# Kernel tuning notes

Hardware: AMD Instinct MI355X
Metric: run time of the kernel (lower is better)

Reference implementation:

```python
import jax, jax.numpy as jnp
import numpy as np

S, T, B = 128, 64, 64          # src_len, trg_len, batch
E, H, D, A, V = 512, 512, 1024, 256, 32000  # emb, enc_hid, dec_hid(=2H), attn, vocab
PAD = 0


def _p(key, shape, scale=0.02):
    return jax.random.normal(key, shape, dtype=jnp.float32) * scale


def setup_inputs() -> dict:
    key = jax.random.key(0)
    ks = jax.random.split(key, 20)
    return {
        'src': jax.random.randint(ks[0], (S, B), 0, V, dtype=jnp.int32),
        'trg': jax.random.randint(ks[1], (T, B), 0, V, dtype=jnp.int32),
        'enc_emb': _p(ks[2], (V, E)),
        'Wf_ih': _p(ks[3], (4 * H, E)), 'Wf_hh': _p(ks[4], (4 * H, H)), 'bf': jnp.zeros((4 * H,), jnp.float32),
        'Wb_ih': _p(ks[5], (4 * H, E)), 'Wb_hh': _p(ks[6], (4 * H, H)), 'bb': jnp.zeros((4 * H,), jnp.float32),
        'Wa': _p(ks[7], (A, 2 * H + D)), 'ba': jnp.zeros((A,), jnp.float32),
        'v': _p(ks[8], (A,)),
        'dec_emb': _p(ks[9], (V, E)),
        'Wd_ih': _p(ks[10], (4 * D, E + 2 * H)), 'Wd_hh': _p(ks[11], (4 * D, D)), 'bd': jnp.zeros((4 * D,), jnp.float32),
        'Wo': _p(ks[12], (V, 2 * H + D + E)), 'bo': jnp.zeros((V,), jnp.float32),
    }


def lstm_cell(x, h, c, W_ih, W_hh, b):
    # PyTorch gate order: i, f, g, o
    g = x @ W_ih.T + h @ W_hh.T + b
    i, f, gg, o = jnp.split(g, 4, axis=-1)
    c2 = jax.nn.sigmoid(f) * c + jax.nn.sigmoid(i) * jnp.tanh(gg)
    h2 = jax.nn.sigmoid(o) * jnp.tanh(c2)
    return h2, c2


def seq2seq_fwd(src, trg, enc_emb, Wf_ih, Wf_hh, bf, Wb_ih, Wb_hh, bb,
                Wa, ba, v, dec_emb, Wd_ih, Wd_hh, bd, Wo, bo):
    emb = enc_emb[src]                                   # [S,B,E]
    z = jnp.zeros((B, H), emb.dtype)

    def fstep(carry, x):
        h, c = lstm_cell(x, *carry, Wf_ih, Wf_hh, bf)
        return (h, c), h

    def bstep(carry, x):
        h, c = lstm_cell(x, *carry, Wb_ih, Wb_hh, bb)
        return (h, c), h

    (hf, cf), hs_f = jax.lax.scan(fstep, (z, z), emb)
    (hb, cb), hs_b = jax.lax.scan(bstep, (z, z), emb[::-1])
    enc_out = jnp.concatenate([hs_f, hs_b[::-1]], axis=-1)   # [S,B,2H]

    h0 = jnp.concatenate([hf, hb], axis=-1)              # [B,D]
    c0 = jnp.concatenate([cf, cb], axis=-1)

    mask = (src != PAD).T                                # [B,S]
    enc_bse = enc_out.transpose(1, 0, 2)                 # [B,S,2H]

    def dstep(carry, tok):
        h, c = carry
        emb_t = dec_emb[tok]                             # [B,E]
        hrep = jnp.broadcast_to(h[:, None, :], (B, S, D))
        energy = jnp.tanh(jnp.concatenate([hrep, enc_bse], -1) @ Wa.T + ba)  # [B,S,A]
        scores = energy @ v                              # [B,S]
        scores = jnp.where(mask, scores, jnp.float32(-1e10))
        a = jax.nn.softmax(scores, axis=1)
        ctx = jnp.einsum('bs,bse->be', a, enc_bse)       # [B,2H]
        x = jnp.concatenate([emb_t, ctx], axis=-1)
        h2, c2 = lstm_cell(x, h, c, Wd_ih, Wd_hh, bd)
        pred = jnp.concatenate([h2, ctx, emb_t], -1) @ Wo.T + bo  # [B,V]
        return (h2, c2), pred

    # teacher_forcing_ratio = 1.0 -> input at step t is trg[t-1]
    _, preds = jax.lax.scan(dstep, (h0, c0), trg[:-1])
    outputs = jnp.concatenate([jnp.zeros((1, B, V), preds.dtype), preds], axis=0)
    return outputs                                       # [T,B,V]


def reference(src, trg, enc_emb, Wf_ih, Wf_hh, bf, Wb_ih, Wb_hh, bb,
              Wa, ba, v, dec_emb, Wd_ih, Wd_hh, bd, Wo, bo):
    return seq2seq_fwd(src, trg, enc_emb, Wf_ih, Wf_hh, bf, Wb_ih, Wb_hh, bb,
                       Wa, ba, v, dec_emb, Wd_ih, Wd_hh, bd, Wo, bo)
```

## Files before the change

kernel.cpp:

```cpp
#include <hip/hip_runtime.h>

#define SLEN  128
#define BATCH 64
#define EMB   512
#define HID   512
#define DDEC  1024
#define ATT   256
#define VOC   32000
#define TSTEPS 63
#define SLOT  1024

typedef _Float16 f16x4 __attribute__((ext_vector_type(4)));
typedef _Float16 f16x8 __attribute__((ext_vector_type(8)));
typedef float    f32x4 __attribute__((ext_vector_type(4)));

union HQ  { unsigned long long q[2]; f16x8 v; };
union HP  { _Float16 h[2]; unsigned u; };
union HP4 { _Float16 h[4]; f16x4 v4; unsigned long long u; };

__device__ __forceinline__ float sigmoidf_(float x) { return 1.0f / (1.0f + __expf(-x)); }
__device__ __forceinline__ float tanhf_(float x)    { return 1.0f - 2.0f / (__expf(2.0f * x) + 1.0f); }

__device__ __forceinline__ void st_u32(void* p, unsigned v) {
    __hip_atomic_store((unsigned*)p, v, __ATOMIC_RELAXED, __HIP_MEMORY_SCOPE_AGENT);
}
__device__ __forceinline__ void st_u64(void* p, unsigned long long v) {
    __hip_atomic_store((unsigned long long*)p, v, __ATOMIC_RELAXED, __HIP_MEMORY_SCOPE_AGENT);
}
__device__ __forceinline__ unsigned long long ld_u64(const void* p) {
    return __hip_atomic_load((const unsigned long long*)p, __ATOMIC_RELAXED, __HIP_MEMORY_SCOPE_AGENT);
}
__device__ __forceinline__ void st_i32(int* p, int v) {
    __hip_atomic_store(p, v, __ATOMIC_RELAXED, __HIP_MEMORY_SCOPE_AGENT);
}
__device__ __forceinline__ int ld_i32(const int* p) {
    return __hip_atomic_load(p, __ATOMIC_RELAXED, __HIP_MEMORY_SCOPE_AGENT);
}

__device__ __forceinline__ void bar_arrive(int* flags, int myid, int epoch) {
    __syncthreads();
    if (threadIdx.x == 0) st_i32(flags + myid * SLOT, epoch);
}
__device__ __forceinline__ void bar_wait(int* flags, int nf, int epoch) {
    if ((int)threadIdx.x < 64) {
        bool done = false;
        while (!done) {
            bool ok = true;
            for (int i = threadIdx.x; i < nf; i += 64)
                ok = ok && (ld_i32(flags + i * SLOT) >= epoch);
            done = __all(ok);
            if (!done) __builtin_amdgcn_s_sleep(1);
        }
    }
    __syncthreads();
}

__global__ __launch_bounds__(256) void init_convert(
    const int* __restrict__ src, const int* __restrict__ trg,
    const float* __restrict__ enc_emb, const float* __restrict__ dec_emb,
    const float* __restrict__ Wf_ih, const float* __restrict__ Wf_hh,
    const float* __restrict__ Wb_ih, const float* __restrict__ Wb_hh,
    const float* __restrict__ Wa, const float* __restrict__ Wd_ih, const float* __restrict__ Wd_hh,
    float* __restrict__ out0,
    _Float16* __restrict__ Wenc16, _Float16* __restrict__ Wd16, _Float16* __restrict__ Wa16,
    _Float16* __restrict__ emb_src16, _Float16* __restrict__ predA,
    float* __restrict__ c_enc, _Float16* __restrict__ h16_enc, int* __restrict__ bar_ws)
{
    long idx = (long)blockIdx.x * 256 + threadIdx.x;
    if (idx < 2048000L) { out0[idx] = 0.f; return; }
    idx -= 2048000L;
    if (idx < 4194304L) {
        int dir = (int)(idx >> 21);
        int rem = (int)(idx & ((1 << 21) - 1));
        int rr = rem >> 10, c = rem & 1023;
        int d = rr >> 2, qg = rr & 3;
        const float* Wih = dir ? Wb_ih : Wf_ih;
        const float* Whh = dir ? Wb_hh : Wf_hh;
        float v = (c < 512) ? Wih[(long)(qg * 512 + d) * 512 + c]
                            : Whh[(long)(qg * 512 + d) * 512 + (c - 512)];
        Wenc16[idx] = (_Float16)v; return;
    }
    idx -= 4194304L;
    if (idx < 10485760L) {
        int rr = (int)(idx / 2560), c = (int)(idx % 2560);
        int d = rr >> 2, qg = rr & 3;
        float v = (c < 1536) ? Wd_ih[(long)(qg * 1024 + d) * 1536 + c]
                             : Wd_hh[(long)(qg * 1024 + d) * 1024 + (c - 1536)];
        Wd16[idx] = (_Float16)v; return;
    }
    idx -= 10485760L;
    if (idx < 262144L) {
        int rr = (int)(idx >> 10), c = (int)(idx & 1023);
        Wa16[idx] = (_Float16)Wa[(long)rr * 2048 + c]; return;
    }
    idx -= 262144L;
    if (idx < 4194304L) {
        int sb = (int)(idx >> 9), e = (int)(idx & 511);
        int tok = src[sb];
        emb_src16[idx] = (_Float16)enc_emb[(long)tok * 512 + e]; return;
    }
    idx -= 4194304L;
    if (idx < 2064384L) {
        int rI = (int)(idx >> 9), e = (int)(idx & 511);
        int tok = trg[rI];
        predA[(long)(64 + rI) * 2560 + 2048 + e] = (_Float16)dec_emb[(long)tok * 512 + e]; return;
    }
    idx -= 2064384L;
    if (idx < 65536L) { c_enc[idx] = 0.f; return; }
    idx -= 65536L;
    if (idx < 65536L) { h16_enc[idx] = (_Float16)0.f; return; }
    idx -= 65536L;
    if (idx < 655360L) { bar_ws[idx] = 0; }
}

__global__ __launch_bounds__(256, 1) void enc_coop(
    const _Float16* __restrict__ Wenc16, const _Float16* __restrict__ emb_src16,
    _Float16* __restrict__ h16_enc, float* __restrict__ c_enc,
    const float* __restrict__ bf, const float* __restrict__ bb,
    _Float16* __restrict__ enc_out16, int* __restrict__ bar_ws)
{
    __shared__ _Float16 Wl[32768];
    __shared__ float gbuf[32][34];

    const int t = threadIdx.x, lane = t & 63, wv = t >> 6;
    const int blk = blockIdx.x;
    const int g = blk >> 6, wb = blk & 63;
    const int dir = g >> 1, bh = g & 1;
    const int r16 = lane & 15, kg = lane >> 4;
    int* eflags = bar_ws + (384 + g * 64) * SLOT;

    #pragma unroll
    for (int i = 0; i < 16; ++i) {
        int h0 = (i * 256 + t) * 8;
        int kc = h0 >> 10;
        int rem = h0 & 1023;
        int gt2 = rem >> 9, l = (rem >> 3) & 63;
        f16x8 v = *(const f16x8*)(Wenc16 +
            ((size_t)(dir * 2048 + wb * 32 + gt2 * 16 + (l & 15))) * 1024 + (l >> 4) * 8 + kc * 32);
        *(f16x8*)&Wl[h0] = v;
    }

    const float* bias = dir ? bb : bf;
    const int pb = t & 31, dp = t >> 5;
    const int dl0 = dp * 2;
    float bias2[2][4], creg2[2] = {0.f, 0.f};
    if (t < 128) {
        #pragma unroll
        for (int j = 0; j < 2; ++j)
            #pragma unroll
            for (int q = 0; q < 4; ++q)
                bias2[j][q] = bias[q * 512 + wb * 8 + dl0 + j];
    }
    __syncthreads();

    for (int s = 0; s < SLEN; ++s) {
        const int par = s & 1;
        const int s_eff = dir ? (127 - s) : s;
        const int gt = wv & 1, mb = wv >> 1;
        const int arow = bh * 32 + mb * 16 + r16;
        const _Float16* Ax = emb_src16 + ((size_t)(s_eff * 64 + arow)) * 512 + kg * 8;
        const unsigned long long* Hq =
            (const unsigned long long*)(h16_enc + ((size_t)((par * 2 + dir) * 64 + arow)) * 512);
        f32x4 acc = {};
        #pragma unroll 4
        for (int kc = 0; kc < 16; ++kc) {
            f16x8 bw = *(const f16x8*)&Wl[kc * 1024 + gt * 512 + lane * 8];
            f16x8 a  = *(const f16x8*)(Ax + kc * 32);
            acc = __builtin_amdgcn_mfma_f32_16x16x32_f16(a, bw, acc, 0, 0, 0);
        }
        #pragma unroll 4
        for (int kc = 0; kc < 16; ++kc) {
            f16x8 bw = *(const f16x8*)&Wl[(16 + kc) * 1024 + gt * 512 + lane * 8];
            HQ hq;
            hq.q[0] = ld_u64(Hq + kc * 8 + kg * 2);
            hq.q[1] = ld_u64(Hq + kc * 8 + kg * 2 + 1);
            acc = __builtin_amdgcn_mfma_f32_16x16x32_f16(hq.v, bw, acc, 0, 0, 0);
        }
        #pragma unroll
        for (int rI = 0; rI < 4; ++rI)
            gbuf[gt * 16 + (lane & 15)][mb * 16 + kg * 4 + rI] = acc[rI];
        __syncthreads();
        if (t < 128) {
            HP hp;
            #pragma unroll
            for (int j = 0; j < 2; ++j) {
                const int dl = dl0 + j;
                float g0 = gbuf[dl * 4 + 0][pb] + bias2[j][0];
                float g1 = gbuf[dl * 4 + 1][pb] + bias2[j][1];
                float g2 = gbuf[dl * 4 + 2][pb] + bias2[j][2];
                float g3 = gbuf[dl * 4 + 3][pb] + bias2[j][3];
                float c2 = sigmoidf_(g1) * creg2[j] + sigmoidf_(g0) * tanhf_(g2);
                float h2 = sigmoidf_(g3) * tanhf_(c2);
                creg2[j] = c2;
                hp.h[j] = (_Float16)h2;
            }
            const int bglob = bh * 32 + pb;
            const int d0 = wb * 8 + dl0;
            st_u32((void*)(h16_enc + ((size_t)((par ^ 1) * 2 + dir) * 64 + bglob) * 512 + d0), hp.u);
            *(unsigned*)(enc_out16 + ((size_t)s_eff * 64 + bglob) * 1024 + dir * 512 + d0) = hp.u;
        }
        bar_arrive(eflags, wb, s + 1);
        bar_wait(eflags, 64, s + 1);
    }
    if (t < 128) {
        const int bglob = bh * 32 + pb;
        const int d0 = wb * 8 + dl0;
        c_enc[((size_t)dir * 64 + bglob) * 512 + d0] = creg2[0];
        c_enc[((size_t)dir * 64 + bglob) * 512 + d0 + 1] = creg2[1];
    }
}

__global__ __launch_bounds__(256, 1) void dec_coop(
    const _Float16* __restrict__ Wd16, const _Float16* __restrict__ Wa16,
    const float* __restrict__ bd, const float* __restrict__ vvec,
    const int* __restrict__ src, const _Float16* __restrict__ enc_part16,
    const _Float16* __restrict__ enc_out16, const float* __restrict__ c_enc,
    _Float16* __restrict__ predA, int* __restrict__ bar_ws)
{
    __shared__ float gbuf[16][68];
    __shared__ float ha[256], sv[256], sc[128], esum[256], red[4];

    const int t = threadIdx.x, lane = t & 63, wv = t >> 6;
    const int r16 = lane & 15, kg = lane >> 4;
    const int blk = blockIdx.x;
    int* cf  = bar_ws;
    int* hs  = bar_ws + 64 * SLOT;
    int* hf0 = bar_ws + 320 * SLOT;

    if (blk < 64) {
        const int wb = blk;
        sv[t] = vvec[t];
        {
            const int d0 = t * 4;
            const size_t rbase = (d0 < 512) ? (size_t)(127 * 64 + wb) * 1024
                                            : (size_t)(0 * 64 + wb) * 1024;
            HP4 o;
            o.h[0] = enc_out16[rbase + d0];
            o.h[1] = enc_out16[rbase + d0 + 1];
            o.h[2] = enc_out16[rbase + d0 + 2];
            o.h[3] = enc_out16[rbase + d0 + 3];
            st_u64((void*)(predA + (size_t)wb * 2560 + d0), o.u);
        }
        bar_arrive(hf0, wb, 1);
        for (int tt = 0; tt < TSTEPS; ++tt) {
            if (tt == 0) bar_wait(hf0, 64, 1); else bar_wait(hs, 256, tt);
            {
                const int base_m = wb & 48;
                const _Float16* Ahh = predA + ((size_t)(tt * 64 + base_m + r16)) * 2560 + kg * 8;
                f32x4 acc4[4] = {};
                #pragma unroll 4
                for (int kc = 0; kc < 32; ++kc) {
                    f16x8 a = *(const f16x8*)(Ahh + kc * 32);
                    #pragma unroll
                    for (int jj = 0; jj < 4; ++jj) {
                        f16x8 bw = *(const f16x8*)(Wa16 +
                            ((size_t)((wv * 4 + jj) * 16 + r16)) * 1024 + kg * 8 + kc * 32);
                        acc4[jj] = __builtin_amdgcn_mfma_f32_16x16x32_f16(a, bw, acc4[jj], 0, 0, 0);
                    }
                }
                if (kg == ((wb & 15) >> 2)) {
                    #pragma unroll
                    for (int jj = 0; jj < 4; ++jj)
                        ha[(wv * 4 + jj) * 16 + r16] = acc4[jj][wb & 3];
                }
            }
            __syncthreads();
            {
                const int s = t & 127, jh = t >> 7;
                const f16x8* ep = (const f16x8*)(enc_part16 + ((size_t)s * 64 + wb) * 256 + jh * 128);
                float acc = 0.f;
                #pragma unroll 2
                for (int j8 = 0; j8 < 16; ++j8) {
                    f16x8 e = ep[j8];
                    #pragma unroll
                    for (int u = 0; u < 8; ++u)
                        acc += tanhf_(ha[jh * 128 + j8 * 8 + u] + (float)e[u]) * sv[jh * 128 + j8 * 8 + u];
                }
                esum[t] = acc;
            }
            __syncthreads();
            if (t < 128) {
                float scv = esum[t] + esum[128 + t];
                scv = (src[t * 64 + wb] != 0) ? scv : -1e10f;
                sc[t] = scv;
                float v = scv;
                #pragma unroll
                for (int off = 32; off > 0; off >>= 1) v = fmaxf(v, __shfl_xor(v, off));
                if (lane == 0) red[t >> 6] = v;
            }
            __syncthreads();
            {
                const float mx = fmaxf(red[0], red[1]);
                if (t < 128) {
                    float e = __expf(sc[t] - mx);
                    sc[t] = e;
                    float v = e;
                    #pragma unroll
                    for (int off = 32; off > 0; off >>= 1) v += __shfl_xor(v, off);
                    if (lane == 0) red[2 + (t >> 6)] = v;
                }
            }
            __syncthreads();
            {
                const float inv = 1.0f / (red[2] + red[3]);
                float a0 = 0.f, a1 = 0.f, a2 = 0.f, a3 = 0.f;
                #pragma unroll 4
                for (int sI = 0; sI < 128; ++sI) {
                    float as = sc[sI] * inv;
                    f16x4 ev = *(const f16x4*)(enc_out16 + ((size_t)sI * 64 + wb) * 1024 + t * 4);
                    a0 += as * (float)ev[0]; a1 += as * (float)ev[1];
                    a2 += as * (float)ev[2]; a3 += as * (float)ev[3];
                }
                HP4 o;
                o.h[0] = (_Float16)a0; o.h[1] = (_Float16)a1;
                o.h[2] = (_Float16)a2; o.h[3] = (_Float16)a3;
                st_u64((void*)(predA + ((size_t)(64 + tt * 64 + wb)) * 2560 + 1024 + t * 4), o.u);
            }
            bar_arrive(cf, wb, tt + 1);
        }
    } else {
        const int gid = blk - 64;
        const int pb = t & 63;
        float bias2[2][4], creg2[2] = {0.f, 0.f};
        if (t < 128) {
            #pragma unroll
            for (int j = 0; j < 2; ++j) {
                const int dg = gid * 4 + (t >> 6) * 2 + j;
                #pragma unroll
                for (int q = 0; q < 4; ++q) bias2[j][q] = bd[q * 1024 + dg];
                creg2[j] = (dg < 512) ? c_enc[(size_t)pb * 512 + dg]
                                      : c_enc[(size_t)(64 + pb) * 512 + (dg - 512)];
            }
        }
        const _Float16* Bbase = Wd16 + (size_t)(gid * 16 + r16) * 2560 + kg * 8;
        for (int tt = 0; tt < TSTEPS; ++tt) {
            if (tt == 0) bar_wait(hf0, 64, 1); else bar_wait(hs, 256, tt);
            const int mb = wv;
            const _Float16* Ae = predA + ((size_t)(64 + tt * 64 + mb * 16 + r16)) * 2560 + kg * 8;
            const _Float16* Ah = predA + ((size_t)(tt * 64 + mb * 16 + r16)) * 2560 + kg * 8;
            f32x4 acc = {};
            #pragma unroll 4
            for (int kc = 0; kc < 16; ++kc) {
                f16x8 bw = *(const f16x8*)(Bbase + kc * 32);
                f16x8 a  = *(const f16x8*)(Ae + 2048 + kc * 32);
                acc = __builtin_amdgcn_mfma_f32_16x16x32_f16(a, bw, acc, 0, 0, 0);
            }
            #pragma unroll 4
            for (int kc = 0; kc < 32; ++kc) {
                f16x8 bw = *(const f16x8*)(Bbase + 1536 + kc * 32);
                f16x8 a  = *(const f16x8*)(Ah + kc * 32);
                acc = __builtin_amdgcn_mfma_f32_16x16x32_f16(a, bw, acc, 0, 0, 0);
            }
            bar_wait(cf, 64, tt + 1);
            #pragma unroll 4
            for (int kc = 0; kc < 32; ++kc) {
                f16x8 bw = *(const f16x8*)(Bbase + 512 + kc * 32);
                f16x8 a  = *(const f16x8*)(Ae + 1024 + kc * 32);
                acc = __builtin_amdgcn_mfma_f32_16x16x32_f16(a, bw, acc, 0, 0, 0);
            }
            #pragma unroll
            for (int rI = 0; rI < 4; ++rI)
                gbuf[lane & 15][mb * 16 + kg * 4 + rI] = acc[rI];
            __syncthreads();
            if (t < 128) {
                HP hp;
                #pragma unroll
                for (int j = 0; j < 2; ++j) {
                    const int dl = (t >> 6) * 2 + j;
                    float g0 = gbuf[dl * 4 + 0][pb] + bias2[j][0];
                    float g1 = gbuf[dl * 4 + 1][pb] + bias2[j][1];
                    float g2 = gbuf[dl * 4 + 2][pb] + bias2[j][2];
                    float g3 = gbuf[dl * 4 + 3][pb] + bias2[j][3];
                    float c2 = sigmoidf_(g1) * creg2[j] + sigmoidf_(g0) * tanhf_(g2);
                    float h2 = sigmoidf_(g3) * tanhf_(c2);
                    creg2[j] = c2;
                    hp.h[j] = (_Float16)h2;
                }
                st_u32((void*)(predA + ((size_t)(64 + tt * 64 + pb)) * 2560 + gid * 4 + (t >> 6) * 2), hp.u);
            }
            bar_arrive(hs, gid, tt + 1);
        }
    }
}

__global__ __launch_bounds__(64) void enc_step_mfma(
    const _Float16* __restrict__ Wenc16, const _Float16* __restrict__ emb_src16,
    _Float16* __restrict__ h16_enc, float* __restrict__ c_enc,
    const float* __restrict__ bf, const float* __restrict__ bb,
    _Float16* __restrict__ enc_out16, int s)
{
    __shared__ float gbuf[16 * 66];
    const int lane = threadIdx.x;
    const int blk = blockIdx.x;
    const int dir = blk >> 7, tile = blk & 127;
    const int par = s & 1;
    const int s_eff = dir ? (SLEN - 1 - s) : s;
    const int r16 = lane & 15, kg = lane >> 4;

    const _Float16* Bw = Wenc16 + ((size_t)(dir * 2048 + tile * 16 + r16)) * 1024 + kg * 8;
    const _Float16* Ax = emb_src16 + ((size_t)(s_eff * 64 + r16)) * 512 + kg * 8;
    const _Float16* Ah = h16_enc + ((size_t)((par * 2 + dir) * 64 + r16)) * 512 + kg * 8;

    f32x4 acc[4] = {};
    #pragma unroll 4
    for (int kc = 0; kc < 16; ++kc) {
        f16x8 bfr = *(const f16x8*)(Bw + kc * 32);
        #pragma unroll
        for (int m = 0; m < 4; ++m) {
            f16x8 a = *(const f16x8*)(Ax + kc * 32 + (size_t)m * 16 * 512);
            acc[m] = __builtin_amdgcn_mfma_f32_16x16x32_f16(a, bfr, acc[m], 0, 0, 0);
        }
    }
    #pragma unroll 4
    for (int kc = 0; kc < 16; ++kc) {
        f16x8 bfr = *(const f16x8*)(Bw + 512 + kc * 32);
        #pragma unroll
        for (int m = 0; m < 4; ++m) {
            f16x8 a = *(const f16x8*)(Ah + kc * 32 + (size_t)m * 16 * 512);
            acc[m] = __builtin_amdgcn_mfma_f32_16x16x32_f16(a, bfr, acc[m], 0, 0, 0);
        }
    }
    #pragma unroll
    for (int m = 0; m < 4; ++m)
        #pragma unroll
        for (int rI = 0; rI < 4; ++rI)
            gbuf[r16 * 66 + m * 16 + kg * 4 + rI] = acc[m][rI];
    __syncthreads();

    const float* bias = dir ? bb : bf;
    const int b = lane;
    #pragma unroll
    for (int dl = 0; dl < 4; ++dl) {
        const int d = tile * 4 + dl;
        float g0 = gbuf[(dl * 4 + 0) * 66 + b] + bias[d];
        float g1 = gbuf[(dl * 4 + 1) * 66 + b] + bias[512 + d];
        float g2 = gbuf[(dl * 4 + 2) * 66 + b] + bias[1024 + d];
        float g3 = gbuf[(dl * 4 + 3) * 66 + b] + bias[1536 + d];
        const size_t cur = ((size_t)(par * 2 + dir) * 64 + b) * 512 + d;
        const size_t nxt = ((size_t)((par ^ 1) * 2 + dir) * 64 + b) * 512 + d;
        float c2 = sigmoidf_(g1) * c_enc[cur] + sigmoidf_(g0) * tanhf_(g2);
        float h2 = sigmoidf_(g3) * tanhf_(c2);
        c_enc[nxt] = c2;
        h16_enc[nxt] = (_Float16)h2;
        enc_out16[((size_t)s_eff * 64 + b) * 1024 + dir * 512 + d] = (_Float16)h2;
    }
}

__global__ __launch_bounds__(256) void dec_init(
    const _Float16* __restrict__ enc_out16, const float* __restrict__ c_enc,
    _Float16* __restrict__ predA, float* __restrict__ c_dec)
{
    int idx = blockIdx.x * 256 + threadIdx.x;
    int b = (idx >> 10) & 63, d = idx & 1023;
    if (idx < 65536) {
        _Float16 v = (d < 512) ? enc_out16[(size_t)(127 * 64 + b) * 1024 + d]
                               : enc_out16[(size_t)(0 * 64 + b) * 1024 + d];
        predA[(size_t)b * 2560 + d] = v;
    } else {
        float v = (d < 512) ? c_enc[((size_t)(0 * 2 + 0) * 64 + b) * 512 + d]
                            : c_enc[((size_t)(0 * 2 + 1) * 64 + b) * 512 + (d - 512)];
        c_dec[(size_t)b * 1024 + d] = v;
    }
}

__global__ __launch_bounds__(64) void hatt_mfma(
    const _Float16* __restrict__ predA, const _Float16* __restrict__ Wa16,
    float* __restrict__ hatt, int t)
{
    const int lane = threadIdx.x;
    const int tile = blockIdx.x;
    const int r16 = lane & 15, kg = lane >> 4;
    const _Float16* Ap = predA + ((size_t)(t * 64 + r16)) * 2560 + kg * 8;
    const _Float16* Bw = Wa16 + ((size_t)(tile * 16 + r16)) * 1024 + kg * 8;
    f32x4 acc[4] = {};
    #pragma unroll 4
    for (int kc = 0; kc < 32; ++kc) {
        f16x8 bfr = *(const f16x8*)(Bw + kc * 32);
        #pragma unroll
        for (int m = 0; m < 4; ++m) {
            f16x8 a = *(const f16x8*)(Ap + kc * 32 + (size_t)m * 16 * 2560);
            acc[m] = __builtin_amdgcn_mfma_f32_16x16x32_f16(a, bfr, acc[m], 0, 0, 0);
        }
    }
    #pragma unroll
    for (int m = 0; m < 4; ++m)
        #pragma unroll
        for (int rI = 0; rI < 4; ++rI)
            hatt[(size_t)(m * 16 + kg * 4 + rI) * 256 + tile * 16 + r16] = acc[m][rI];
}

__global__ __launch_bounds__(256) void attn_step(
    const int* __restrict__ src, const float* __restrict__ hatt, const float* __restrict__ vvec,
    const _Float16* __restrict__ enc_part16, const _Float16* __restrict__ enc_out16,
    _Float16* __restrict__ predA, int t)
{
    __shared__ float ha[256], sv[256], sc[128], red[128];
    const int b = blockIdx.x, tid = threadIdx.x;
    ha[tid] = hatt[b * 256 + tid];
    sv[tid] = vvec[tid];
    __syncthreads();
    if (tid < 128) {
        const f16x8* ep = (const f16x8*)(enc_part16 + ((size_t)tid * 64 + b) * 256);
        float acc = 0.f;
        #pragma unroll 4
        for (int j8 = 0; j8 < 32; ++j8) {
            f16x8 e = ep[j8];
            #pragma unroll
            for (int u = 0; u < 8; ++u)
                acc += tanhf_(ha[j8 * 8 + u] + (float)e[u]) * sv[j8 * 8 + u];
        }
        float scv = (src[tid * 64 + b] != 0) ? acc : -1e10f;
        sc[tid] = scv; red[tid] = scv;
    }
    __syncthreads();
    for (int off = 64; off > 0; off >>= 1) { if (tid < off) red[tid] = fmaxf(red[tid], red[tid + off]); __syncthreads(); }
    const float mx = red[0];
    __syncthreads();
    if (tid < 128) { float e = __expf(sc[tid] - mx); sc[tid] = e; red[tid] = e; }
    __syncthreads();
    for (int off = 64; off > 0; off >>= 1) { if (tid < off) red[tid] += red[tid + off]; __syncthreads(); }
    const float inv = 1.0f / red[0];
    __syncthreads();

    float a0 = 0.f, a1 = 0.f, a2 = 0.f, a3 = 0.f;
    for (int sI = 0; sI < 128; ++sI) {
        float as = sc[sI] * inv;
        f16x4 ev = *(const f16x4*)(enc_out16 + ((size_t)sI * 64 + b) * 1024 + tid * 4);
        a0 += as * (float)ev[0]; a1 += as * (float)ev[1];
        a2 += as * (float)ev[2]; a3 += as * (float)ev[3];
    }
    f16x4 o = { (_Float16)a0, (_Float16)a1, (_Float16)a2, (_Float16)a3 };
    *(f16x4*)(predA + ((size_t)(64 + t * 64 + b)) * 2560 + 1024 + tid * 4) = o;
}

__global__ __launch_bounds__(64) void dec_gates(
    const _Float16* __restrict__ Wd16, const float* __restrict__ bd,
    float* __restrict__ c_dec, _Float16* __restrict__ predA, int t)
{
    __shared__ float gbuf[16 * 66];
    const int lane = threadIdx.x;
    const int tile = blockIdx.x;
    const int par = t & 1;
    const int r16 = lane & 15, kg = lane >> 4;
    const _Float16* Bw = Wd16 + ((size_t)(tile * 16 + r16)) * 2560 + kg * 8;
    const _Float16* At = predA + ((size_t)(64 + t * 64 + r16)) * 2560 + kg * 8;
    const _Float16* Ah = predA + ((size_t)(t * 64 + r16)) * 2560 + kg * 8;
    f32x4 acc[4] = {};
    #pragma unroll 4
    for (int kc = 0; kc < 16; ++kc) {
        f16x8 bfr = *(const f16x8*)(Bw + kc * 32);
        #pragma unroll
        for (int m = 0; m < 4; ++m) {
            f16x8 a = *(const f16x8*)(At + 2048 + kc * 32 + (size_t)m * 16 * 2560);
            acc[m] = __builtin_amdgcn_mfma_f32_16x16x32_f16(a, bfr, acc[m], 0, 0, 0);
        }
    }
    #pragma unroll 4
    for (int kc = 0; kc < 32; ++kc) {
        f16x8 bfr = *(const f16x8*)(Bw + 512 + kc * 32);
        #pragma unroll
        for (int m = 0; m < 4; ++m) {
            f16x8 a = *(const f16x8*)(At + 1024 + kc * 32 + (size_t)m * 16 * 2560);
            acc[m] = __builtin_amdgcn_mfma_f32_16x16x32_f16(a, bfr, acc[m], 0, 0, 0);
        }
    }
    #pragma unroll 4
    for (int kc = 0; kc < 32; ++kc) {
        f16x8 bfr = *(const f16x8*)(Bw + 1536 + kc * 32);
        #pragma unroll
        for (int m = 0; m < 4; ++m) {
            f16x8 a = *(const f16x8*)(Ah + kc * 32 + (size_t)m * 16 * 2560);
            acc[m] = __builtin_amdgcn_mfma_f32_16x16x32_f16(a, bfr, acc[m], 0, 0, 0);
        }
    }
    #pragma unroll
    for (int m = 0; m < 4; ++m)
        #pragma unroll
        for (int rI = 0; rI < 4; ++rI)
            gbuf[r16 * 66 + m * 16 + kg * 4 + rI] = acc[m][rI];
    __syncthreads();

    const int b = lane;
    #pragma unroll
    for (int dl = 0; dl < 4; ++dl) {
        const int d = tile * 4 + dl;
        float g0 = gbuf[(dl * 4 + 0) * 66 + b] + bd[d];
        float g1 = gbuf[(dl * 4 + 1) * 66 + b] + bd[1024 + d];
        float g2 = gbuf[(dl * 4 + 2) * 66 + b] + bd[2048 + d];
        float g3 = gbuf[(dl * 4 + 3) * 66 + b] + bd[3072 + d];
        float c2 = sigmoidf_(g1) * c_dec[(size_t)(par * 64 + b) * 1024 + d] + sigmoidf_(g0) * tanhf_(g2);
        float h2 = sigmoidf_(g3) * tanhf_(c2);
        c_dec[(size_t)((par ^ 1) * 64 + b) * 1024 + d] = c2;
        predA[((size_t)(64 + t * 64 + b)) * 2560 + d] = (_Float16)h2;
    }
}

__global__ __launch_bounds__(256, 2) void gemm_a16(
    const _Float16* __restrict__ A, int lda,
    const float* __restrict__ B, int ldb,
    const float* __restrict__ bias,
    void* __restrict__ Cv, int ldc, int K, int Mvalid, int ntn, int c16)
{
    __shared__ _Float16 As[8192];
    __shared__ _Float16 Bs[8192];

    const int nwg = gridDim.x;
    const int id = blockIdx.x;
    const int q = nwg >> 3, r = nwg & 7;
    const int xcd = id & 7, ix = id >> 3;
    const int wg = (xcd < r) ? (xcd * (q + 1) + ix) : (r * (q + 1) + (xcd - r) * q + ix);
    const int per = ntn << 3;
    const int g = wg / per, rem = wg % per;
    const int mt = g * 8 + (rem & 7), nt = rem >> 3;

    const int t = threadIdx.x, lane = t & 63, wid = t >> 6;
    const int wr = wid >> 1, wc = wid & 1;

    const int arow_s = t >> 3, ac8 = t & 7;
    const int brow_s = t >> 4, bc4 = t & 15;
    const _Float16* Ap = A + (size_t)(mt * 128 + arow_s) * lda + ac8 * 8;
    const float*    Bp = B + (size_t)(nt * 128 + brow_s) * ldb + bc4 * 4;
    const int awx = (ac8 * 8) ^ ((arow_s & 7) << 3);
    const int bwx = (bc4 * 4) ^ ((brow_s & 7) << 3);

    const int kts = K >> 6;
    f32x4 acc[4][4] = {};
    f16x8 ra[4]; float4 rb[8];
    #pragma unroll
    for (int i = 0; i < 4; ++i) ra[i] = *(const f16x8*)(Ap + (size_t)i * 32 * lda);
    #pragma unroll
    for (int i = 0; i < 8; ++i) rb[i] = *(const float4*)(Bp + (size_t)i * 16 * ldb);

    const int abase = (wr * 64 + (lane & 15)) * 64 + (lane >> 4) * 8;
    const int bbase = (wc * 64 + (lane & 15)) * 64 + (lane >> 4) * 8;
    const int sxor = (lane & 7) << 3;

    for (int kt = 0; kt < kts; ++kt) {
        f16x4 cb[8];
        #pragma unroll
        for (int i = 0; i < 8; ++i)
            cb[i] = (f16x4){(_Float16)rb[i].x, (_Float16)rb[i].y, (_Float16)rb[i].z, (_Float16)rb[i].w};
        __syncthreads();
        #pragma unroll
        for (int i = 0; i < 4; ++i)
            *(f16x8*)&As[(arow_s + i * 32) * 64 + awx] = ra[i];
        #pragma unroll
        for (int i = 0; i < 8; ++i)
            *(f16x4*)&Bs[(brow_s + i * 16) * 64 + bwx] = cb[i];
        __syncthreads();
        if (kt + 1 < kts) {
            #pragma unroll
            for (int i = 0; i < 4; ++i) ra[i] = *(const f16x8*)(Ap + (size_t)i * 32 * lda + (kt + 1) * 64);
            #pragma unroll
            for (int i = 0; i < 8; ++i) rb[i] = *(const float4*)(Bp + (size_t)i * 16 * ldb + (kt + 1) * 64);
        }
        #pragma unroll
        for (int kk = 0; kk < 2; ++kk) {
            f16x8 af[4], bfr[4];
            #pragma unroll
            for (int m = 0; m < 4; ++m) af[m]  = *(const f16x8*)&As[(abase + m * 16 * 64 + kk * 32) ^ sxor];
            #pragma unroll
            for (int n = 0; n < 4; ++n) bfr[n] = *(const f16x8*)&Bs[(bbase + n * 16 * 64 + kk * 32) ^ sxor];
            #pragma unroll
            for (int m = 0; m < 4; ++m)
                #pragma unroll
                for (int n = 0; n < 4; ++n)
                    acc[m][n] = __builtin_amdgcn_mfma_f32_16x16x32_f16(af[m], bfr[n], acc[m][n], 0, 0, 0);
        }
    }

    const int ccol = nt * 128 + wc * 64 + (lane & 15);
    const int crow0 = mt * 128 + wr * 64 + ((lane >> 4) << 2);
    float bv[4];
    #pragma unroll
    for (int n = 0; n < 4; ++n) bv[n] = bias[ccol + n * 16];
    #pragma unroll
    for (int m = 0; m < 4; ++m) {
        #pragma unroll
        for (int rI = 0; rI < 4; ++rI) {
            const int row = crow0 + m * 16 + rI;
            if (row < Mvalid) {
                if (c16) {
                    _Float16* C = (_Float16*)Cv;
                    #pragma unroll
                    for (int n = 0; n < 4; ++n)
                        C[(size_t)row * ldc + ccol + n * 16] = (_Float16)(acc[m][n][rI] + bv[n]);
                } else {
                    float* C = (float*)Cv;
                    #pragma unroll
                    for (int n = 0; n < 4; ++n)
                        C[(size_t)row * ldc + ccol + n * 16] = acc[m][n][rI] + bv[n];
                }
            }
        }
    }
}

extern "C" void kernel_launch(void* const* d_in, const int* in_sizes, int n_in,
                              void* d_out, int out_size, void* d_ws, size_t ws_size,
                              hipStream_t stream) {
    const int*   src     = (const int*)d_in[0];
    const int*   trg     = (const int*)d_in[1];
    const float* enc_emb = (const float*)d_in[2];
    const float* Wf_ih   = (const float*)d_in[3];
    const float* Wf_hh   = (const float*)d_in[4];
    const float* bf      = (const float*)d_in[5];
    const float* Wb_ih   = (const float*)d_in[6];
    const float* Wb_hh   = (const float*)d_in[7];
    const float* bb      = (const float*)d_in[8];
    const float* Wa      = (const float*)d_in[9];
    const float* ba      = (const float*)d_in[10];
    const float* vvec    = (const float*)d_in[11];
    const float* dec_emb = (const float*)d_in[12];
    const float* Wd_ih   = (const float*)d_in[13];
    const float* Wd_hh   = (const float*)d_in[14];
    const float* bd      = (const float*)d_in[15];
    const float* Wo      = (const float*)d_in[16];
    const float* bo      = (const float*)d_in[17];
    float* out = (float*)d_out;

    char* w = (char*)d_ws;
    _Float16* Wenc16     = (_Float16*)(w);
    _Float16* Wd16       = (_Float16*)(w + 8388608);
    _Float16* Wa16       = (_Float16*)(w + 29360128);
    _Float16* emb_src16  = (_Float16*)(w + 29884416);
    _Float16* enc_out16  = (_Float16*)(w + 38273024);
    _Float16* predA      = (_Float16*)(w + 55050240);
    _Float16* h16_enc    = (_Float16*)(w + 76349440);
    float*    c_enc      = (float*)   (w + 76611584);
    float*    c_dec      = (float*)   (w + 77135872);
    float*    hatt       = (float*)   (w + 77660160);
    _Float16* enc_part16 = (_Float16*)(w + 77725696);
    int*      bar_ws     = (int*)     (w + 81920000);
    const size_t need_bytes = 84541440;
    if (ws_size < need_bytes) return;

    init_convert<<<93888, 256, 0, stream>>>(
        src, trg, enc_emb, dec_emb, Wf_ih, Wf_hh, Wb_ih, Wb_hh, Wa, Wd_ih, Wd_hh,
        out, Wenc16, Wd16, Wa16, emb_src16, predA, c_enc, h16_enc, bar_ws);

    {
        const _Float16* a0 = Wenc16; const _Float16* a1 = emb_src16;
        _Float16* a2 = h16_enc; float* a3 = c_enc;
        const float* a4 = bf; const float* a5 = bb;
        _Float16* a6 = enc_out16; int* a7 = bar_ws;
        void* args[] = { &a0, &a1, &a2, &a3, &a4, &a5, &a6, &a7 };
        hipError_t e = hipLaunchCooperativeKernel((const void*)enc_coop, dim3(256), dim3(256), args, 0, stream);
        if (e != hipSuccess) {
            for (int s = 0; s < SLEN; ++s)
                enc_step_mfma<<<256, 64, 0, stream>>>(Wenc16, emb_src16, h16_enc, c_enc, bf, bb, enc_out16, s);
        }
    }

    gemm_a16<<<128, 256, 0, stream>>>(enc_out16, 1024, Wa + 1024, 2048, ba,
                                      enc_part16, 256, 1024, 8192, 2, 1);

    {
        const _Float16* a0 = Wd16; const _Float16* a1 = Wa16;
        const float* a2 = bd; const float* a3 = vvec;
        const int* a4 = src; const _Float16* a5 = enc_part16;
        const _Float16* a6 = enc_out16; const float* a7 = c_enc;
        _Float16* a8 = predA; int* a9 = bar_ws;
        void* args[] = { &a0, &a1, &a2, &a3, &a4, &a5, &a6, &a7, &a8, &a9 };
        hipError_t e = hipLaunchCooperativeKernel((const void*)dec_coop, dim3(320), dim3(256), args, 0, stream);
        if (e != hipSuccess) {
            dec_init<<<512, 256, 0, stream>>>(enc_out16, c_enc, predA, c_dec);
            for (int t = 0; t < TSTEPS; ++t) {
                hatt_mfma<<<16, 64, 0, stream>>>(predA, Wa16, hatt, t);
                attn_step<<<64, 256, 0, stream>>>(src, hatt, vvec, enc_part16, enc_out16, predA, t);
                dec_gates<<<256, 64, 0, stream>>>(Wd16, bd, c_dec, predA, t);
            }
        }
    }

    gemm_a16<<<8000, 256, 0, stream>>>(predA + (size_t)64 * 2560, 2560, Wo, 2560, bo,
                                       out + (size_t)64 * VOC, VOC, 2560, 4032, 250, 0);
}
```

Before: 6.228 ms.

## Merge attention and gate blocks into 256 blocks with LDS-resident decoder weights

The decoder cooperative kernel drops from 320 blocks (64 attention plus 256 gate blocks) to 256 blocks. Blocks 0-63 now run the attention step and then also a gate tile each step. Each block preloads its 16-row slice of the decoder LSTM weights (80 KB of fp16) into LDS once, so the per-step weight reads come from shared memory instead of global or L2. This removes repeated weight traffic in the recurrence, but the first 64 blocks now do attention and gate work in sequence, which lengthens their step. The large LDS allocation also limits each CU to one block.

```diff
diff --git a/kernel.cpp b/kernel.cpp
--- a/kernel.cpp
+++ b/kernel.cpp
@@ -217,33 +217,63 @@
     const _Float16* __restrict__ enc_out16, const float* __restrict__ c_enc,
     _Float16* __restrict__ predA, int* __restrict__ bar_ws)
 {
+    __shared__ _Float16 Wl[40960];
     __shared__ float gbuf[16][68];
     __shared__ float ha[256], sv[256], sc[128], esum[256], red[4];
 
     const int t = threadIdx.x, lane = t & 63, wv = t >> 6;
     const int r16 = lane & 15, kg = lane >> 4;
     const int blk = blockIdx.x;
+    const int gid = blk;
     int* cf  = bar_ws;
     int* hs  = bar_ws + 64 * SLOT;
     int* hf0 = bar_ws + 320 * SLOT;
 
+    #pragma unroll
+    for (int i = 0; i < 20; ++i) {
+        int h0 = (i * 256 + t) * 8;
+        int kc = h0 >> 9, l = (h0 >> 3) & 63;
+        f16x8 v = *(const f16x8*)(Wd16 + ((size_t)(gid * 16 + (l & 15))) * 2560 + (l >> 4) * 8 + kc * 32);
+        *(f16x8*)&Wl[h0] = v;
+    }
+
+    const int pb = t & 63;
+    const int dl0 = (t >> 6) * 2;
+    float bias2[2][4], creg2[2] = {0.f, 0.f};
+    if (t < 128) {
+        #pragma unroll
+        for (int j = 0; j < 2; ++j) {
+            const int dg = gid * 4 + dl0 + j;
+            #pragma unroll
+            for (int q = 0; q < 4; ++q) bias2[j][q] = bd[q * 1024 + dg];
+            creg2[j] = (dg < 512) ? c_enc[(size_t)pb * 512 + dg]
+                                  : c_enc[(size_t)(64 + pb) * 512 + (dg - 512)];
+        }
+    }
+
     if (blk < 64) {
-        const int wb = blk;
         sv[t] = vvec[t];
         {
             const int d0 = t * 4;
-            const size_t rbase = (d0 < 512) ? (size_t)(127 * 64 + wb) * 1024
-                                            : (size_t)(0 * 64 + wb) * 1024;
+            const size_t rbase = (d0 < 512) ? (size_t)(127 * 64 + blk) * 1024
+                                            : (size_t)(0 * 64 + blk) * 1024;
             HP4 o;
             o.h[0] = enc_out16[rbase + d0];
             o.h[1] = enc_out16[rbase + d0 + 1];
             o.h[2] = enc_out16[rbase + d0 + 2];
             o.h[3] = enc_out16[rbase + d0 + 3];
-            st_u64((void*)(predA + (size_t)wb * 2560 + d0), o.u);
-        }
-        bar_arrive(hf0, wb, 1);
-        for (int tt = 0; tt < TSTEPS; ++tt) {
-            if (tt == 0) bar_wait(hf0, 64, 1); else bar_wait(hs, 256, tt);
+            st_u64((void*)(predA + (size_t)blk * 2560 + d0), o.u);
+        }
+        bar_arrive(hf0, blk, 1);
+    } else {
+        __syncthreads();
+    }
+
+    for (int tt = 0; tt < TSTEPS; ++tt) {
+        if (tt == 0) bar_wait(hf0, 64, 1); else bar_wait(hs, 256, tt);
+
+        if (blk < 64) {
+            const int wb = blk;
             {
                 const int base_m = wb & 48;
                 const _Float16* Ahh = predA + ((size_t)(tt * 64 + base_m + r16)) * 2560 + kg * 8;
@@ -318,68 +348,53 @@
             }
             bar_arrive(cf, wb, tt + 1);
         }
-    } else {
-        const int gid = blk - 64;
-        const int pb = t & 63;
-        float bias2[2][4], creg2[2] = {0.f, 0.f};
-        if (t < 128) {
-            #pragma unroll
-            for (int j = 0; j < 2; ++j) {
-                const int dg = gid * 4 + (t >> 6) * 2 + j;
-                #pragma unroll
-                for (int q = 0; q < 4; ++q) bias2[j][q] = bd[q * 1024 + dg];
-                creg2[j] = (dg < 512) ? c_enc[(size_t)pb * 512 + dg]
-                                      : c_enc[(size_t)(64 + pb) * 512 + (dg - 512)];
-            }
-        }
-        const _Float16* Bbase = Wd16 + (size_t)(gid * 16 + r16) * 2560 + kg * 8;
-        for (int tt = 0; tt < TSTEPS; ++tt) {
-            if (tt == 0) bar_wait(hf0, 64, 1); else bar_wait(hs, 256, tt);
+
+        {
             const int mb = wv;
             const _Float16* Ae = predA + ((size_t)(64 + tt * 64 + mb * 16 + r16)) * 2560 + kg * 8;
             const _Float16* Ah = predA + ((size_t)(tt * 64 + mb * 16 + r16)) * 2560 + kg * 8;
             f32x4 acc = {};
             #pragma unroll 4
             for (int kc = 0; kc < 16; ++kc) {
-                f16x8 bw = *(const f16x8*)(Bbase + kc * 32);
+                f16x8 bw = *(const f16x8*)&Wl[kc * 512 + lane * 8];
                 f16x8 a  = *(const f16x8*)(Ae + 2048 + kc * 32);
                 acc = __builtin_amdgcn_mfma_f32_16x16x32_f16(a, bw, acc, 0, 0, 0);
             }
             #pragma unroll 4
             for (int kc = 0; kc < 32; ++kc) {
-                f16x8 bw = *(const f16x8*)(Bbase + 1536 + kc * 32);
+                f16x8 bw = *(const f16x8*)&Wl[(48 + kc) * 512 + lane * 8];
                 f16x8 a  = *(const f16x8*)(Ah + kc * 32);
                 acc = __builtin_amdgcn_mfma_f32_16x16x32_f16(a, bw, acc, 0, 0, 0);
             }
             bar_wait(cf, 64, tt + 1);
             #pragma unroll 4
             for (int kc = 0; kc < 32; ++kc) {
-                f16x8 bw = *(const f16x8*)(Bbase + 512 + kc * 32);
+                f16x8 bw = *(const f16x8*)&Wl[(16 + kc) * 512 + lane * 8];
                 f16x8 a  = *(const f16x8*)(Ae + 1024 + kc * 32);
                 acc = __builtin_amdgcn_mfma_f32_16x16x32_f16(a, bw, acc, 0, 0, 0);
             }
             #pragma unroll
             for (int rI = 0; rI < 4; ++rI)
                 gbuf[lane & 15][mb * 16 + kg * 4 + rI] = acc[rI];
-            __syncthreads();
-            if (t < 128) {
-                HP hp;
-                #pragma unroll
-                for (int j = 0; j < 2; ++j) {
-                    const int dl = (t >> 6) * 2 + j;
-                    float g0 = gbuf[dl * 4 + 0][pb] + bias2[j][0];
-                    float g1 = gbuf[dl * 4 + 1][pb] + bias2[j][1];
-                    float g2 = gbuf[dl * 4 + 2][pb] + bias2[j][2];
-                    float g3 = gbuf[dl * 4 + 3][pb] + bias2[j][3];
-                    float c2 = sigmoidf_(g1) * creg2[j] + sigmoidf_(g0) * tanhf_(g2);
-                    float h2 = sigmoidf_(g3) * tanhf_(c2);
-                    creg2[j] = c2;
-                    hp.h[j] = (_Float16)h2;
-                }
-                st_u32((void*)(predA + ((size_t)(64 + tt * 64 + pb)) * 2560 + gid * 4 + (t >> 6) * 2), hp.u);
-            }
-            bar_arrive(hs, gid, tt + 1);
-        }
+        }
+        __syncthreads();
+        if (t < 128) {
+            HP hp;
+            #pragma unroll
+            for (int j = 0; j < 2; ++j) {
+                const int dl = dl0 + j;
+                float g0 = gbuf[dl * 4 + 0][pb] + bias2[j][0];
+                float g1 = gbuf[dl * 4 + 1][pb] + bias2[j][1];
+                float g2 = gbuf[dl * 4 + 2][pb] + bias2[j][2];
+                float g3 = gbuf[dl * 4 + 3][pb] + bias2[j][3];
+                float c2 = sigmoidf_(g1) * creg2[j] + sigmoidf_(g0) * tanhf_(g2);
+                float h2 = sigmoidf_(g3) * tanhf_(c2);
+                creg2[j] = c2;
+                hp.h[j] = (_Float16)h2;
+            }
+            st_u32((void*)(predA + ((size_t)(64 + tt * 64 + pb)) * 2560 + gid * 4 + dl0), hp.u);
+        }
+        bar_arrive(hs, gid, tt + 1);
     }
 }
 
@@ -762,7 +777,7 @@
         const _Float16* a6 = enc_out16; const float* a7 = c_enc;
         _Float16* a8 = predA; int* a9 = bar_ws;
         void* args[] = { &a0, &a1, &a2, &a3, &a4, &a5, &a6, &a7, &a8, &a9 };
-        hipError_t e = hipLaunchCooperativeKernel((const void*)dec_coop, dim3(320), dim3(256), args, 0, stream);
+        hipError_t e = hipLaunchCooperativeKernel((const void*)dec_coop, dim3(256), dim3(256), args, 0, stream);
         if (e != hipSuccess) {
             dec_init<<<512, 256, 0, stream>>>(enc_out16, c_enc, predA, c_dec);
             for (int t = 0; t < TSTEPS; ++t) {
```

After: 5.116 ms. -17.8%, faster.
